# Optimization experiments

Hardware: AMD Instinct MI355X
Metric: run time of the kernel (lower is better)

Reference implementation:

```python
import math
import jax, jax.numpy as jnp
import numpy as np


def _pairwise_sqdist(x, y):
    # x: [N, d], y: [M, d] -> [N, M]
    x2 = jnp.sum(x * x, axis=-1)[:, None]
    y2 = jnp.sum(y * y, axis=-1)[None, :]
    return jnp.maximum(x2 + y2 - 2.0 * (x @ y.T), 0.0)


def setup_inputs() -> dict:
    key = jax.random.key(0)
    k1, k2 = jax.random.split(key)
    N, M, D = 8192, 8192, 2
    base_points = jax.random.normal(k1, (N, D), dtype=jnp.float32)
    target_points = jax.random.normal(k2, (M, D), dtype=jnp.float32)
    log_sigma = jnp.asarray(math.log(0.1), dtype=jnp.float32)
    log_scale = jnp.zeros((D,), dtype=jnp.float32)
    return {
        "base_points": base_points,
        "target_points": target_points,
        "log_sigma": log_sigma,
        "log_scale": log_scale,
    }


def reference(base_points, target_points, log_sigma, log_scale):
    # learn_scale=True: anisotropic per-coordinate scaling
    scale = jnp.exp(log_scale)
    base = base_points * scale
    target = target_points * scale

    # uniform node weights (use_weight_net=False)
    N = base.shape[0]
    M = target.shape[0]
    w_base = jnp.full((N,), 1.0 / N, dtype=base.dtype)
    w_target = jnp.full((M,), 1.0 / M, dtype=target.dtype)

    # center=True: subtract weighted centroid of each cloud
    base = base - jnp.sum(w_base[:, None] * base, axis=0, keepdims=True)
    target = target - jnp.sum(w_target[:, None] * target, axis=0, keepdims=True)

    sigma = jnp.exp(log_sigma)
    inv2s2 = 1.0 / (2.0 * sigma * sigma)

    k_bb = jnp.exp(-_pairwise_sqdist(base, base) * inv2s2)      # [N, N]
    k_tt = jnp.exp(-_pairwise_sqdist(target, target) * inv2s2)  # [M, M]
    k_bt = jnp.exp(-_pairwise_sqdist(base, target) * inv2s2)    # [N, M]

    term_bb = w_base @ (k_bb @ w_base)
    term_tt = w_target @ (k_tt @ w_target)
    term_bt = w_base @ (k_bt @ w_target)
    loss = term_bb + term_tt - 2.0 * term_bt
    return loss
```

## Files before the change

### kernel.cpp

```cpp
#include <hip/hip_runtime.h>


#define BLOCK 256
#define GRID  2048
#define LOG2E 1.4426950408889634f
#define MAGIC 0x5ca1ab1eu

__device__ __forceinline__ float fexp2(float x) {
    return __builtin_amdgcn_exp2f(x);
}

__device__ __forceinline__ double tile_plain(const float* __restrict__ tb0,
                                             const float2* __restrict__ tbxy,
                                             float ax2, float ay2, float A0)
{
    const float4* bp = (const float4*)tbxy;
    const float4* cp = (const float4*)tb0;
    float s0 = 0.f, s1 = 0.f, s2 = 0.f, s3 = 0.f;
#pragma unroll 4
    for (int q = 0; q < 64; ++q) {
        float4 pA = bp[2 * q];
        float4 pB = bp[2 * q + 1];
        float4 c  = cp[q];
        float e0 = fmaf(ax2, pA.x, c.x) + fmaf(ay2, pA.y, A0);
        float e1 = fmaf(ax2, pA.z, c.y) + fmaf(ay2, pA.w, A0);
        float e2 = fmaf(ax2, pB.x, c.z) + fmaf(ay2, pB.y, A0);
        float e3 = fmaf(ax2, pB.z, c.w) + fmaf(ay2, pB.w, A0);
        s0 += fexp2(e0); s1 += fexp2(e1);
        s2 += fexp2(e2); s3 += fexp2(e3);
    }
    return (double)((s0 + s1) + (s2 + s3));
}

__device__ __forceinline__ double tile_diag(const float* __restrict__ tb0,
                                            const float2* __restrict__ tbxy,
                                            float ax2, float ay2, float A0,
                                            int row, int j0)
{
    const float4* bp = (const float4*)tbxy;
    const float4* cp = (const float4*)tb0;
    float sge = 0.f, sgt = 0.f;
#pragma unroll 2
    for (int q = 0; q < 64; ++q) {
        float4 pA = bp[2 * q];
        float4 pB = bp[2 * q + 1];
        float4 c  = cp[q];
        float e0 = fmaf(ax2, pA.x, c.x) + fmaf(ay2, pA.y, A0);
        float e1 = fmaf(ax2, pA.z, c.y) + fmaf(ay2, pA.w, A0);
        float e2 = fmaf(ax2, pB.x, c.z) + fmaf(ay2, pB.y, A0);
        float e3 = fmaf(ax2, pB.z, c.w) + fmaf(ay2, pB.w, A0);
        float v0 = fexp2(e0), v1 = fexp2(e1);
        float v2 = fexp2(e2), v3 = fexp2(e3);
        int j = j0 + 4 * q;
        sge += (j + 0 >= row) ? v0 : 0.f;  sgt += (j + 0 > row) ? v0 : 0.f;
        sge += (j + 1 >= row) ? v1 : 0.f;  sgt += (j + 1 > row) ? v1 : 0.f;
        sge += (j + 2 >= row) ? v2 : 0.f;  sgt += (j + 2 > row) ? v2 : 0.f;
        sge += (j + 3 >= row) ? v3 : 0.f;  sgt += (j + 3 > row) ? v3 : 0.f;
    }
    return (double)(sge + sgt);
}

__global__ __launch_bounds__(BLOCK, 8) void mmd_one(
    const float* __restrict__ base, const float* __restrict__ target,
    const float* __restrict__ log_sigma, const float* __restrict__ log_scale,
    int N, int M,
    double* __restrict__ bslot,
    unsigned* __restrict__ flag,
    float* __restrict__ out)
{
    __shared__ __align__(16) float2 tbxy[256];
    __shared__ __align__(16) float  tb0[256];
    __shared__ double wredd[4];
    __shared__ double mred[4][4];
    __shared__ float2 shsh;

    const int tid = threadIdx.x;
    const int bid = blockIdx.x;

    const float s0c   = expf(log_scale[0]);
    const float s1c   = expf(log_scale[1]);
    const float sigma = expf(log_sigma[0]);
    const float inv2s2 = 1.0f / (2.0f * sigma * sigma);
    const float sq = sqrtf(inv2s2 * LOG2E);
    const float f0 = s0c * sq, f1 = s1c * sq;

    const float2* base2   = (const float2*)base;
    const float2* target2 = (const float2*)target;

    const double wNN = 1.0 / ((double)N * (double)N);
    const double wMM = 1.0 / ((double)M * (double)M);
    const double wNM = -2.0 / ((double)N * (double)M);

    double result = 0.0;

    if (bid < 1024) {
        {
            double sbx = 0, sby = 0, stx = 0, sty = 0;
            const float4* b4 = (const float4*)base;
            const float4* t4 = (const float4*)target;
            const int nb4 = N >> 1, nt4 = M >> 1;
            for (int i = tid; i < nb4; i += BLOCK) {
                float4 v = b4[i];
                sbx += (double)v.x + (double)v.z;
                sby += (double)v.y + (double)v.w;
            }
            for (int i = tid; i < nt4; i += BLOCK) {
                float4 v = t4[i];
                stx += (double)v.x + (double)v.z;
                sty += (double)v.y + (double)v.w;
            }
            for (int off = 32; off; off >>= 1) {
                sbx += __shfl_down(sbx, off); sby += __shfl_down(sby, off);
                stx += __shfl_down(stx, off); sty += __shfl_down(sty, off);
            }
            const int w = tid >> 6;
            if ((tid & 63) == 0) {
                mred[w][0] = sbx; mred[w][1] = sby;
                mred[w][2] = stx; mred[w][3] = sty;
            }
            __syncthreads();
            if (tid == 0) {
                double b0 = 0, b1 = 0, t0 = 0, t1 = 0;
                for (int k = 0; k < 4; ++k) {
                    b0 += mred[k][0]; b1 += mred[k][1];
                    t0 += mred[k][2]; t1 += mred[k][3];
                }
                shsh.x = (float)(b0 / (double)N - t0 / (double)M) * f0;
                shsh.y = (float)(b1 / (double)N - t1 / (double)M) * f1;
            }
            __syncthreads();
        }
        const float sh0 = shsh.x, sh1 = shsh.y;

        const int ib = bid >> 5, jb = bid & 31;
        const int i0 = ib * 256, j0 = jb * 256;

        {
            float2 b = target2[j0 + tid];
            float bx = b.x * f0, by = b.y * f1;
            tbxy[tid] = make_float2(bx, by);
            tb0[tid]  = -fmaf(bx, bx, by * by);
        }
        __syncthreads();

        float2 a = base2[i0 + tid];
        const float ax = fmaf(a.x, f0, -sh0);
        const float ay = fmaf(a.y, f1, -sh1);
        const float ax2 = ax + ax, ay2 = ay + ay;
        const float A0 = -fmaf(ax, ax, ay * ay);

        result += wNM * tile_plain(tb0, tbxy, ax2, ay2, A0);
    } else {
        const int v0i = bid - 1024;
        const int npass = (v0i < 32) ? 2 : 1;
        for (int pass = 0; pass < npass; ++pass) {
            const int v = (pass == 0) ? v0i : (v0i + 1024);
            const int term = (v >= 528) ? 1 : 0;
            const int u = v - term * 528;
            int ib = (int)((65.0f - sqrtf(4225.0f - 8.0f * (float)u)) * 0.5f);
            ib = min(max(ib, 0), 31);
            while (ib > 0 && (ib * (65 - ib)) / 2 > u) --ib;
            while (ib < 31 && ((ib + 1) * (64 - ib)) / 2 <= u) ++ib;
            const int jb = ib + (u - (ib * (65 - ib)) / 2);

            const float2* A2 = term ? target2 : base2;
            const double w = term ? wMM : wNN;
            const int i0 = ib * 256, j0 = jb * 256;

            __syncthreads();
            {
                float2 b = A2[j0 + tid];
                float bx = b.x * f0, by = b.y * f1;
                tbxy[tid] = make_float2(bx, by);
                tb0[tid]  = -fmaf(bx, bx, by * by);
            }
            __syncthreads();

            const int row = i0 + tid;
            float2 a = A2[row];
            const float ax = a.x * f0, ay = a.y * f1;
            const float ax2 = ax + ax, ay2 = ay + ay;
            const float A0 = -fmaf(ax, ax, ay * ay);

            if (jb > ib) {
                result += (2.0 * w) * tile_plain(tb0, tbxy, ax2, ay2, A0);
            } else {
                result += w * tile_diag(tb0, tbxy, ax2, ay2, A0, row, j0);
            }
        }
    }

    for (int off = 32; off; off >>= 1) result += __shfl_down(result, off);
    if ((tid & 63) == 0) wredd[tid >> 6] = result;
    __syncthreads();
    if (tid == 0) {
        double s = wredd[0] + wredd[1] + wredd[2] + wredd[3];
        atomicExch((unsigned long long*)&bslot[bid], (unsigned long long)__double_as_longlong(s));
        __threadfence();
        atomicExch(&flag[bid], MAGIC);
    }

    if (bid == GRID - 1) {
        double lsum = 0.0;
        unsigned done = 0;
        int ndone = 0;
        while (ndone < GRID / BLOCK) {
            for (int k = 0; k < GRID / BLOCK; ++k) {
                if (done & (1u << k)) continue;
                const int i = tid + BLOCK * k;
                if (atomicAdd(&flag[i], 0u) == MAGIC) {
                    __threadfence();
                    unsigned long long raw =
                        atomicAdd((unsigned long long*)&bslot[i], 0ull);
                    lsum += __longlong_as_double((long long)raw);
                    done |= 1u << k;
                    ++ndone;
                }
            }
            if (ndone < GRID / BLOCK) __builtin_amdgcn_s_sleep(4);
        }
        for (int off = 32; off; off >>= 1) lsum += __shfl_down(lsum, off);
        if ((tid & 63) == 0) wredd[tid >> 6] = lsum;
        __syncthreads();
        if (tid == 0) {
            out[0] = (float)(wredd[0] + wredd[1] + wredd[2] + wredd[3]);
        }
    }
}

extern "C" void kernel_launch(void* const* d_in, const int* in_sizes, int n_in,
                              void* d_out, int out_size, void* d_ws, size_t ws_size,
                              hipStream_t stream)
{
    const float* base      = (const float*)d_in[0];
    const float* target    = (const float*)d_in[1];
    const float* log_sigma = (const float*)d_in[2];
    const float* log_scale = (const float*)d_in[3];
    float* out = (float*)d_out;

    int N = in_sizes[0] / 2;
    int M = in_sizes[1] / 2;

    double*   bslot = (double*)d_ws;
    unsigned* flag  = (unsigned*)(bslot + GRID);

    mmd_one<<<dim3(GRID), dim3(BLOCK), 0, stream>>>(
        base, target, log_sigma, log_scale, N, M, bslot, flag, out);
}
```

Measured before the change: 110.4 us.

## Split centroid prep into its own kernel and schedule tiles via atomic queue

Centroid and scale computation moves into a single-block prep kernel, so the 1024 cross-term blocks no longer each re-read both point clouds. The main kernel pulls 128x256 half-height tiles from a global atomic work counter, with each thread covering half a column span. A wave-uniform test skips the exp2 evaluation when every exponent in a group of four falls below -40. The spin-wait final reduction is replaced by a double atomicAdd plus a last-block-done counter. In exchange it pays an extra kernel launch and atomic contention on the tile counter, and the skip drops kernel terms below 2^-40, which will rarely fire on scattered inputs.

```diff
diff --git a/kernel.cpp b/kernel.cpp
--- a/kernel.cpp
+++ b/kernel.cpp
@@ -1,89 +1,85 @@
 #include <hip/hip_runtime.h>
 
 
-#define BLOCK 256
-#define GRID  2048
-#define LOG2E 1.4426950408889634f
-#define MAGIC 0x5ca1ab1eu
+#define BLOCK    256
+#define GRID     2048
+#define NT_CROSS 2048
+#define NT_SYM   2112
+#define NT_TOT   (NT_CROSS + NT_SYM)
+#define LOG2E    1.4426950408889634f
+#define SKIP_CUT (-40.0f)
+
+struct Prep { float f0, f1, sh0, sh1; };
 
 __device__ __forceinline__ float fexp2(float x) {
     return __builtin_amdgcn_exp2f(x);
 }
 
-__device__ __forceinline__ double tile_plain(const float* __restrict__ tb0,
-                                             const float2* __restrict__ tbxy,
-                                             float ax2, float ay2, float A0)
-{
-    const float4* bp = (const float4*)tbxy;
-    const float4* cp = (const float4*)tb0;
-    float s0 = 0.f, s1 = 0.f, s2 = 0.f, s3 = 0.f;
-#pragma unroll 4
-    for (int q = 0; q < 64; ++q) {
-        float4 pA = bp[2 * q];
-        float4 pB = bp[2 * q + 1];
-        float4 c  = cp[q];
-        float e0 = fmaf(ax2, pA.x, c.x) + fmaf(ay2, pA.y, A0);
-        float e1 = fmaf(ax2, pA.z, c.y) + fmaf(ay2, pA.w, A0);
-        float e2 = fmaf(ax2, pB.x, c.z) + fmaf(ay2, pB.y, A0);
-        float e3 = fmaf(ax2, pB.z, c.w) + fmaf(ay2, pB.w, A0);
-        s0 += fexp2(e0); s1 += fexp2(e1);
-        s2 += fexp2(e2); s3 += fexp2(e3);
-    }
-    return (double)((s0 + s1) + (s2 + s3));
-}
-
-__device__ __forceinline__ double tile_diag(const float* __restrict__ tb0,
-                                            const float2* __restrict__ tbxy,
-                                            float ax2, float ay2, float A0,
-                                            int row, int j0)
-{
-    const float4* bp = (const float4*)tbxy;
-    const float4* cp = (const float4*)tb0;
-    float sge = 0.f, sgt = 0.f;
-#pragma unroll 2
-    for (int q = 0; q < 64; ++q) {
-        float4 pA = bp[2 * q];
-        float4 pB = bp[2 * q + 1];
-        float4 c  = cp[q];
-        float e0 = fmaf(ax2, pA.x, c.x) + fmaf(ay2, pA.y, A0);
-        float e1 = fmaf(ax2, pA.z, c.y) + fmaf(ay2, pA.w, A0);
-        float e2 = fmaf(ax2, pB.x, c.z) + fmaf(ay2, pB.y, A0);
-        float e3 = fmaf(ax2, pB.z, c.w) + fmaf(ay2, pB.w, A0);
-        float v0 = fexp2(e0), v1 = fexp2(e1);
-        float v2 = fexp2(e2), v3 = fexp2(e3);
-        int j = j0 + 4 * q;
-        sge += (j + 0 >= row) ? v0 : 0.f;  sgt += (j + 0 > row) ? v0 : 0.f;
-        sge += (j + 1 >= row) ? v1 : 0.f;  sgt += (j + 1 > row) ? v1 : 0.f;
-        sge += (j + 2 >= row) ? v2 : 0.f;  sgt += (j + 2 > row) ? v2 : 0.f;
-        sge += (j + 3 >= row) ? v3 : 0.f;  sgt += (j + 3 > row) ? v3 : 0.f;
-    }
-    return (double)(sge + sgt);
-}
-
-__global__ __launch_bounds__(BLOCK, 8) void mmd_one(
+__global__ __launch_bounds__(1024) void prep_kernel(
     const float* __restrict__ base, const float* __restrict__ target,
     const float* __restrict__ log_sigma, const float* __restrict__ log_scale,
+    int N, int M, Prep* __restrict__ pp,
+    unsigned* __restrict__ wctr, unsigned* __restrict__ dctr,
+    double* __restrict__ acc)
+{
+    __shared__ double mred[16][4];
+    const int tid = threadIdx.x;
+    if (tid == 0) { *wctr = 0u; *dctr = 0u; *acc = 0.0; }
+
+    double sbx = 0, sby = 0, stx = 0, sty = 0;
+    const float4* b4 = (const float4*)base;
+    const float4* t4 = (const float4*)target;
+    for (int i = tid; i < (N >> 1); i += 1024) {
+        float4 v = b4[i];
+        sbx += (double)v.x + (double)v.z;
+        sby += (double)v.y + (double)v.w;
+    }
+    for (int i = tid; i < (M >> 1); i += 1024) {
+        float4 v = t4[i];
+        stx += (double)v.x + (double)v.z;
+        sty += (double)v.y + (double)v.w;
+    }
+    for (int off = 32; off; off >>= 1) {
+        sbx += __shfl_down(sbx, off); sby += __shfl_down(sby, off);
+        stx += __shfl_down(stx, off); sty += __shfl_down(sty, off);
+    }
+    if ((tid & 63) == 0) {
+        mred[tid >> 6][0] = sbx; mred[tid >> 6][1] = sby;
+        mred[tid >> 6][2] = stx; mred[tid >> 6][3] = sty;
+    }
+    __syncthreads();
+    if (tid == 0) {
+        double b0 = 0, b1 = 0, t0 = 0, t1 = 0;
+        for (int k = 0; k < 16; ++k) {
+            b0 += mred[k][0]; b1 += mred[k][1];
+            t0 += mred[k][2]; t1 += mred[k][3];
+        }
+        float s0 = expf(log_scale[0]);
+        float s1 = expf(log_scale[1]);
+        float sigma = expf(log_sigma[0]);
+        float inv2s2 = 1.0f / (2.0f * sigma * sigma);
+        float sq = sqrtf(inv2s2 * LOG2E);
+        float f0 = s0 * sq, f1 = s1 * sq;
+        pp->f0 = f0; pp->f1 = f1;
+        pp->sh0 = (float)(b0 / (double)N - t0 / (double)M) * f0;
+        pp->sh1 = (float)(b1 / (double)N - t1 / (double)M) * f1;
+    }
+}
+
+__global__ __launch_bounds__(BLOCK, 8) void mmd_main(
+    const float* __restrict__ base, const float* __restrict__ target,
     int N, int M,
-    double* __restrict__ bslot,
-    unsigned* __restrict__ flag,
-    float* __restrict__ out)
+    const Prep* __restrict__ pp,
+    unsigned* __restrict__ wctr, unsigned* __restrict__ dctr,
+    double* __restrict__ acc, float* __restrict__ out)
 {
     __shared__ __align__(16) float2 tbxy[256];
     __shared__ __align__(16) float  tb0[256];
+    __shared__ int sh_t;
     __shared__ double wredd[4];
-    __shared__ double mred[4][4];
-    __shared__ float2 shsh;
 
     const int tid = threadIdx.x;
-    const int bid = blockIdx.x;
-
-    const float s0c   = expf(log_scale[0]);
-    const float s1c   = expf(log_scale[1]);
-    const float sigma = expf(log_sigma[0]);
-    const float inv2s2 = 1.0f / (2.0f * sigma * sigma);
-    const float sq = sqrtf(inv2s2 * LOG2E);
-    const float f0 = s0c * sq, f1 = s1c * sq;
-
+    const Prep p = *pp;
     const float2* base2   = (const float2*)base;
     const float2* target2 = (const float2*)target;
 
@@ -93,100 +89,99 @@
 
     double result = 0.0;
 
-    if (bid < 1024) {
+    for (;;) {
+        __syncthreads();
+        if (tid == 0) sh_t = (int)atomicAdd(wctr, 1u);
+        __syncthreads();
+        const int t = sh_t;
+        if (t >= NT_TOT) break;
+
+        int ib, jb, term;
+        bool diag;
+        const float2* A2;
+        const float2* B2;
+        double wt;
+        float shx = 0.f, shy = 0.f;
+        if (t < NT_CROSS) {
+            ib = t >> 5; jb = t & 31;
+            A2 = base2; B2 = target2;
+            wt = wNM; diag = false; term = 2;
+            shx = p.sh0; shy = p.sh1;
+        } else {
+            const int u = t - NT_CROSS;
+            term = (u >= 1056) ? 1 : 0;
+            const int v = u - term * 1056;
+            int q = (int)((65.0f - sqrtf(4225.0f - 4.0f * (float)v)) * 0.5f);
+            q = min(max(q, 0), 31);
+            while (q > 0 && (65 * q - q * q) > v) --q;
+            while (q < 31 && (65 * (q + 1) - (q + 1) * (q + 1)) <= v) ++q;
+            const int r = v - (65 * q - q * q);
+            const int cnt = 32 - q;
+            ib = 2 * q + (r >= cnt ? 1 : 0);
+            jb = q + (r >= cnt ? r - cnt : r);
+            diag = (jb == q);
+            A2 = term ? target2 : base2;  B2 = A2;
+            wt = 2.0 * (term ? wMM : wNN);
+        }
+        const int i0 = ib * 128, j0 = jb * 256;
+
         {
-            double sbx = 0, sby = 0, stx = 0, sty = 0;
-            const float4* b4 = (const float4*)base;
-            const float4* t4 = (const float4*)target;
-            const int nb4 = N >> 1, nt4 = M >> 1;
-            for (int i = tid; i < nb4; i += BLOCK) {
-                float4 v = b4[i];
-                sbx += (double)v.x + (double)v.z;
-                sby += (double)v.y + (double)v.w;
-            }
-            for (int i = tid; i < nt4; i += BLOCK) {
-                float4 v = t4[i];
-                stx += (double)v.x + (double)v.z;
-                sty += (double)v.y + (double)v.w;
-            }
-            for (int off = 32; off; off >>= 1) {
-                sbx += __shfl_down(sbx, off); sby += __shfl_down(sby, off);
-                stx += __shfl_down(stx, off); sty += __shfl_down(sty, off);
-            }
-            const int w = tid >> 6;
-            if ((tid & 63) == 0) {
-                mred[w][0] = sbx; mred[w][1] = sby;
-                mred[w][2] = stx; mred[w][3] = sty;
-            }
-            __syncthreads();
-            if (tid == 0) {
-                double b0 = 0, b1 = 0, t0 = 0, t1 = 0;
-                for (int k = 0; k < 4; ++k) {
-                    b0 += mred[k][0]; b1 += mred[k][1];
-                    t0 += mred[k][2]; t1 += mred[k][3];
-                }
-                shsh.x = (float)(b0 / (double)N - t0 / (double)M) * f0;
-                shsh.y = (float)(b1 / (double)N - t1 / (double)M) * f1;
-            }
-            __syncthreads();
-        }
-        const float sh0 = shsh.x, sh1 = shsh.y;
-
-        const int ib = bid >> 5, jb = bid & 31;
-        const int i0 = ib * 256, j0 = jb * 256;
-
-        {
-            float2 b = target2[j0 + tid];
-            float bx = b.x * f0, by = b.y * f1;
+            float2 b = B2[j0 + tid];
+            float bx = b.x * p.f0, by = b.y * p.f1;
             tbxy[tid] = make_float2(bx, by);
             tb0[tid]  = -fmaf(bx, bx, by * by);
         }
         __syncthreads();
 
-        float2 a = base2[i0 + tid];
-        const float ax = fmaf(a.x, f0, -sh0);
-        const float ay = fmaf(a.y, f1, -sh1);
+        const int row = i0 + (tid & 127);
+        const int js  = (tid >> 7) * 128;
+        float2 a = A2[row];
+        const float ax = fmaf(a.x, p.f0, -shx);
+        const float ay = fmaf(a.y, p.f1, -shy);
         const float ax2 = ax + ax, ay2 = ay + ay;
         const float A0 = -fmaf(ax, ax, ay * ay);
-
-        result += wNM * tile_plain(tb0, tbxy, ax2, ay2, A0);
-    } else {
-        const int v0i = bid - 1024;
-        const int npass = (v0i < 32) ? 2 : 1;
-        for (int pass = 0; pass < npass; ++pass) {
-            const int v = (pass == 0) ? v0i : (v0i + 1024);
-            const int term = (v >= 528) ? 1 : 0;
-            const int u = v - term * 528;
-            int ib = (int)((65.0f - sqrtf(4225.0f - 8.0f * (float)u)) * 0.5f);
-            ib = min(max(ib, 0), 31);
-            while (ib > 0 && (ib * (65 - ib)) / 2 > u) --ib;
-            while (ib < 31 && ((ib + 1) * (64 - ib)) / 2 <= u) ++ib;
-            const int jb = ib + (u - (ib * (65 - ib)) / 2);
-
-            const float2* A2 = term ? target2 : base2;
-            const double w = term ? wMM : wNN;
-            const int i0 = ib * 256, j0 = jb * 256;
-
-            __syncthreads();
-            {
-                float2 b = A2[j0 + tid];
-                float bx = b.x * f0, by = b.y * f1;
-                tbxy[tid] = make_float2(bx, by);
-                tb0[tid]  = -fmaf(bx, bx, by * by);
+        const float4* bp = (const float4*)(tbxy + js);
+        const float4* cp = (const float4*)(tb0 + js);
+
+        if (!diag) {
+            float s0 = 0.f, s1 = 0.f, s2 = 0.f, s3 = 0.f;
+#pragma unroll 4
+            for (int q = 0; q < 32; ++q) {
+                float4 pA = bp[2 * q];
+                float4 pB = bp[2 * q + 1];
+                float4 c  = cp[q];
+                float e0 = fmaf(ax2, pA.x, c.x) + fmaf(ay2, pA.y, A0);
+                float e1 = fmaf(ax2, pA.z, c.y) + fmaf(ay2, pA.w, A0);
+                float e2 = fmaf(ax2, pB.x, c.z) + fmaf(ay2, pB.y, A0);
+                float e3 = fmaf(ax2, pB.z, c.w) + fmaf(ay2, pB.w, A0);
+                float m = fmaxf(fmaxf(e0, e1), fmaxf(e2, e3));
+                if (__any(m > SKIP_CUT)) {
+                    s0 += fexp2(e0); s1 += fexp2(e1);
+                    s2 += fexp2(e2); s3 += fexp2(e3);
+                }
             }
-            __syncthreads();
-
-            const int row = i0 + tid;
-            float2 a = A2[row];
-            const float ax = a.x * f0, ay = a.y * f1;
-            const float ax2 = ax + ax, ay2 = ay + ay;
-            const float A0 = -fmaf(ax, ax, ay * ay);
-
-            if (jb > ib) {
-                result += (2.0 * w) * tile_plain(tb0, tbxy, ax2, ay2, A0);
-            } else {
-                result += w * tile_diag(tb0, tbxy, ax2, ay2, A0, row, j0);
+            result += wt * (double)((s0 + s1) + (s2 + s3));
+        } else {
+            float sge = 0.f, sgt = 0.f;
+            const int jbase = j0 + js;
+#pragma unroll 2
+            for (int q = 0; q < 32; ++q) {
+                float4 pA = bp[2 * q];
+                float4 pB = bp[2 * q + 1];
+                float4 c  = cp[q];
+                float e0 = fmaf(ax2, pA.x, c.x) + fmaf(ay2, pA.y, A0);
+                float e1 = fmaf(ax2, pA.z, c.y) + fmaf(ay2, pA.w, A0);
+                float e2 = fmaf(ax2, pB.x, c.z) + fmaf(ay2, pB.y, A0);
+                float e3 = fmaf(ax2, pB.z, c.w) + fmaf(ay2, pB.w, A0);
+                float v0 = fexp2(e0), v1 = fexp2(e1);
+                float v2 = fexp2(e2), v3 = fexp2(e3);
+                const int j = jbase + 4 * q;
+                sge += (j + 0 >= row) ? v0 : 0.f;  sgt += (j + 0 > row) ? v0 : 0.f;
+                sge += (j + 1 >= row) ? v1 : 0.f;  sgt += (j + 1 > row) ? v1 : 0.f;
+                sge += (j + 2 >= row) ? v2 : 0.f;  sgt += (j + 2 > row) ? v2 : 0.f;
+                sge += (j + 3 >= row) ? v3 : 0.f;  sgt += (j + 3 > row) ? v3 : 0.f;
             }
+            result += (term ? wMM : wNN) * (double)(sge + sgt);
         }
     }
 
@@ -195,35 +190,12 @@
     __syncthreads();
     if (tid == 0) {
         double s = wredd[0] + wredd[1] + wredd[2] + wredd[3];
-        atomicExch((unsigned long long*)&bslot[bid], (unsigned long long)__double_as_longlong(s));
+        atomicAdd(acc, s);
         __threadfence();
-        atomicExch(&flag[bid], MAGIC);
-    }
-
-    if (bid == GRID - 1) {
-        double lsum = 0.0;
-        unsigned done = 0;
-        int ndone = 0;
-        while (ndone < GRID / BLOCK) {
-            for (int k = 0; k < GRID / BLOCK; ++k) {
-                if (done & (1u << k)) continue;
-                const int i = tid + BLOCK * k;
-                if (atomicAdd(&flag[i], 0u) == MAGIC) {
-                    __threadfence();
-                    unsigned long long raw =
-                        atomicAdd((unsigned long long*)&bslot[i], 0ull);
-                    lsum += __longlong_as_double((long long)raw);
-                    done |= 1u << k;
-                    ++ndone;
-                }
-            }
-            if (ndone < GRID / BLOCK) __builtin_amdgcn_s_sleep(4);
-        }
-        for (int off = 32; off; off >>= 1) lsum += __shfl_down(lsum, off);
-        if ((tid & 63) == 0) wredd[tid >> 6] = lsum;
-        __syncthreads();
-        if (tid == 0) {
-            out[0] = (float)(wredd[0] + wredd[1] + wredd[2] + wredd[3]);
+        unsigned d = atomicAdd(dctr, 1u);
+        if (d == (unsigned)(gridDim.x - 1)) {
+            double tot = atomicAdd(acc, 0.0);
+            out[0] = (float)tot;
         }
     }
 }
@@ -241,9 +213,13 @@
     int N = in_sizes[0] / 2;
     int M = in_sizes[1] / 2;
 
-    double*   bslot = (double*)d_ws;
-    unsigned* flag  = (unsigned*)(bslot + GRID);
-
-    mmd_one<<<dim3(GRID), dim3(BLOCK), 0, stream>>>(
-        base, target, log_sigma, log_scale, N, M, bslot, flag, out);
-}
+    Prep*     pp   = (Prep*)d_ws;
+    unsigned* wctr = (unsigned*)((char*)d_ws + 16);
+    unsigned* dctr = (unsigned*)((char*)d_ws + 20);
+    double*   acc  = (double*)((char*)d_ws + 32);
+
+    prep_kernel<<<1, 1024, 0, stream>>>(base, target, log_sigma, log_scale,
+                                        N, M, pp, wctr, dctr, acc);
+    mmd_main<<<GRID, BLOCK, 0, stream>>>(base, target, N, M,
+                                         pp, wctr, dctr, acc, out);
+}
```

Result: slower. 186.7 us (+69.1%).
